# Kernel tuning notes

Hardware: AMD Instinct MI355X
Metric: run time of the kernel (lower is better)

The kernel has to match this reference:

```python
import jax, jax.numpy as jnp
import numpy as np

D = 512        # model dim
NH = 8         # heads
NL = 4         # layers
MSL = 2048     # max_seq_len for relative positional bias
ITEM_V, CATE_V, SEG_V = 100000, 1000, 2
EPS = 1e-5


def layer_norm(x, w, b):
    mu = jnp.mean(x, axis=-1, keepdims=True)
    var = jnp.mean((x - mu) ** 2, axis=-1, keepdims=True)
    return (x - mu) * jax.lax.rsqrt(var + EPS) * w + b


def setup_inputs() -> dict:
    key = jax.random.key(0)
    ks = jax.random.split(key, 16)
    B, L = 8, 1023
    inp = {
        'historical_item_ids': jax.random.randint(ks[0], (B, L), 0, ITEM_V, dtype=jnp.int32),
        'historical_cate_ids': jax.random.randint(ks[1], (B, L), 0, CATE_V, dtype=jnp.int32),
        'historical_len': jax.random.randint(ks[2], (B,), 0, L, dtype=jnp.int32),
        'target_item_id': jax.random.randint(ks[3], (B,), 0, ITEM_V, dtype=jnp.int32),
        'target_cate_id': jax.random.randint(ks[4], (B,), 0, CATE_V, dtype=jnp.int32),
        # embeddings (init std 0.02 like _init_weights)
        'item_emb': 0.02 * jax.random.normal(ks[5], (ITEM_V, D), jnp.float32),
        'cate_emb': 0.02 * jax.random.normal(ks[6], (CATE_V, D), jnp.float32),
        'seg_emb': 0.02 * jax.random.normal(ks[7], (SEG_V, D), jnp.float32),
        # per-layer stacked params
        'W1': 0.02 * jax.random.normal(ks[8], (NL, D, 4 * D), jnp.float32),
        'b1': jnp.zeros((NL, 4 * D), jnp.float32),
        'W2': 0.02 * jax.random.normal(ks[9], (NL, D, D), jnp.float32),
        'b2': jnp.zeros((NL, D), jnp.float32),
        'ln1_w': jnp.ones((NL, D), jnp.float32), 'ln1_b': jnp.zeros((NL, D), jnp.float32),
        'ln2_w': jnp.ones((NL, D), jnp.float32), 'ln2_b': jnp.zeros((NL, D), jnp.float32),
        'pos_w': 0.02 * jax.random.normal(ks[10], (NL, 2 * MSL - 1), jnp.float32),
        'lnf_w': jnp.ones((D,), jnp.float32), 'lnf_b': jnp.zeros((D,), jnp.float32),
    }
    return inp


def _forward(historical_item_ids, historical_cate_ids, historical_len,
             target_item_id, target_cate_id,
             item_emb, cate_emb, seg_emb, W1, b1, W2, b2,
             ln1_w, ln1_b, ln2_w, ln2_b, pos_w, lnf_w, lnf_b):
    B = historical_item_ids.shape[0]
    ar = jnp.arange(B)
    pad = jnp.zeros((B, 1), historical_item_ids.dtype)
    ids = jnp.concatenate([historical_item_ids, pad], axis=1).at[ar, historical_len].set(target_item_id)
    cids = jnp.concatenate([historical_cate_ids, pad], axis=1).at[ar, historical_len].set(target_cate_id)
    S = ids.shape[1]
    seg = jnp.zeros_like(ids).at[ar, historical_len].set(1)

    h = item_emb[ids] + cate_emb[cids] + seg_emb[seg]  # [B,S,D]

    # relative position bias indices: bias[i,j] = pos_w[MSL-1 + j - i]
    rel_idx = MSL - 1 + jnp.arange(S)[None, :] - jnp.arange(S)[:, None]  # [S,S]
    causal = jnp.tril(jnp.ones((S, S), h.dtype))  # multiplicative mask (mask >= 0)

    for l in range(NL):
        z = jax.nn.silu(h @ W1[l] + b1[l])  # [B,S,4D]
        u, q, k, v = jnp.split(z, 4, axis=-1)
        resh = lambda t: t.reshape(B, S, NH, D // NH).transpose(0, 2, 1, 3)  # [B,H,S,hd]
        u, q, k, v = resh(u), resh(q), resh(k), resh(v)
        bias = pos_w[l][rel_idx]  # [S,S]
        att = jax.nn.silu(jnp.einsum('bhsd,bhtd->bhst', q, k) + bias) * causal
        y = jnp.einsum('bhst,bhtd->bhsd', att, v) * u
        y = y.transpose(0, 2, 1, 3).reshape(B, S, D)
        y = layer_norm(y, ln1_w[l], ln1_b[l])
        y = y @ W2[l] + b2[l]
        h = layer_norm(y + h, ln2_w[l], ln2_b[l])  # dropout p=0 (eval)

    return layer_norm(h, lnf_w, lnf_b)


def reference(historical_item_ids, historical_cate_ids, historical_len,
              target_item_id, target_cate_id,
              item_emb, cate_emb, seg_emb, W1, b1, W2, b2,
              ln1_w, ln1_b, ln2_w, ln2_b, pos_w, lnf_w, lnf_b):
    return _forward(historical_item_ids, historical_cate_ids, historical_len,
                    target_item_id, target_cate_id,
                    item_emb, cate_emb, seg_emb, W1, b1, W2, b2,
                    ln1_w, ln1_b, ln2_w, ln2_b, pos_w, lnf_w, lnf_b)
```

## Files before the change

kernel.cpp:

```cpp
#include <hip/hip_runtime.h>
#include <cstddef>


#define D_MODEL 512
#define S_LEN 1024
#define NHEADS 8

typedef __bf16 bf16x8 __attribute__((ext_vector_type(8)));
typedef float f32x4 __attribute__((ext_vector_type(4)));
typedef unsigned short us4 __attribute__((ext_vector_type(4)));
typedef unsigned short us8 __attribute__((ext_vector_type(8)));

__device__ __forceinline__ float silu_f(float x) {
  return x / (1.f + __expf(-x));
}
__device__ __forceinline__ unsigned short f2bf(float f) {
  unsigned int u = __float_as_uint(f);
  u += 0x7FFF + ((u >> 16) & 1);
  return (unsigned short)(u >> 16);
}
__device__ __forceinline__ float bf2f(unsigned short s) {
  return __uint_as_float(((unsigned int)s) << 16);
}
__device__ __forceinline__ void gll16(const void* g, void* l) {
  __builtin_amdgcn_global_load_lds(
      (const __attribute__((address_space(1))) unsigned int*)g,
      (__attribute__((address_space(3))) unsigned int*)l, 16, 0, 0);
}

__global__ __launch_bounds__(256) void embed_kernel(
    const int* __restrict__ hist_i, const int* __restrict__ hist_c,
    const int* __restrict__ hlen, const int* __restrict__ tgt_i,
    const int* __restrict__ tgt_c, const float* __restrict__ item_emb,
    const float* __restrict__ cate_emb, const float* __restrict__ seg_emb,
    float* __restrict__ h32, unsigned short* __restrict__ hbf) {
  int bs = blockIdx.x;
  int b = bs >> 10, s = bs & 1023;
  int l = hlen[b];
  int id, cid, sg;
  if (s == l)       { id = tgt_i[b]; cid = tgt_c[b]; sg = 1; }
  else if (s < 1023){ id = hist_i[b * 1023 + s]; cid = hist_c[b * 1023 + s]; sg = 0; }
  else              { id = 0; cid = 0; sg = 0; }
  const float* ie = item_emb + (size_t)id * D_MODEL;
  const float* ce = cate_emb + (size_t)cid * D_MODEL;
  const float* se = seg_emb + (size_t)sg * D_MODEL;
  float* hr = h32 + (size_t)bs * D_MODEL;
  unsigned short* hb = hbf + (size_t)bs * D_MODEL;
  for (int d = threadIdx.x; d < D_MODEL; d += 256) {
    float v = ie[d] + ce[d] + se[d];
    hr[d] = v;
    hb[d] = f2bf(v);
  }
}

__global__ __launch_bounds__(256) void transpose_kernel(
    const float* __restrict__ W, unsigned short* __restrict__ Wt,
    int K, int N) {
  const int l = blockIdx.z;
  W += (size_t)l * K * N;
  Wt += (size_t)l * K * N;
  const int n0 = blockIdx.x * 64, k0 = blockIdx.y * 64;
  __shared__ float T[64][65];
  const int tid = threadIdx.x;
  const int rr = tid >> 4, cc = (tid & 15) * 4;
#pragma unroll
  for (int p = 0; p < 4; p++) {
    const int r = rr + p * 16;
    const float4 v = *reinterpret_cast<const float4*>(&W[(size_t)(k0 + r) * N + n0 + cc]);
    T[r][cc] = v.x; T[r][cc + 1] = v.y; T[r][cc + 2] = v.z; T[r][cc + 3] = v.w;
  }
  __syncthreads();
#pragma unroll
  for (int p = 0; p < 4; p++) {
    const int r = rr + p * 16;
    us4 o = { f2bf(T[cc + 0][r]), f2bf(T[cc + 1][r]),
              f2bf(T[cc + 2][r]), f2bf(T[cc + 3][r]) };
    *reinterpret_cast<us4*>(&Wt[(size_t)(n0 + r) * K + k0 + cc]) = o;
  }
}

template <int TM, int TN, int SWZ, int EPI_SILU, typename OutT>
__global__ __launch_bounds__(256) void mfma_gemm(
    const unsigned short* __restrict__ A, const unsigned short* __restrict__ Bt,
    const float* __restrict__ bias, OutT* __restrict__ C,
    int M, int N, int K) {
  constexpr int MI = TM / 32, NI = TN / 32;
  __shared__ unsigned short As[TM * 64];
  __shared__ unsigned short Bs[TN * 64];
  const int tid = threadIdx.x;
  const int w = tid >> 6, lane = tid & 63, lm = lane & 15, quad = lane >> 4;
  const int wm = w & 1, wn = w >> 1;
  int m0, n0;
  if (SWZ) {
    const int id = blockIdx.x;
    const int xcd = id & 7, j = id >> 3;
    m0 = (xcd * 4 + (j & 3)) * TM;
    n0 = (j >> 2) * TN;
  } else {
    m0 = blockIdx.y * TM;
    n0 = blockIdx.x * TN;
  }

  f32x4 acc[MI][NI] = {};

  for (int k0 = 0; k0 < K; k0 += 64) {
#pragma unroll
    for (int p = 0; p < TM / 32; p++) {
      const int g = p * 256 + tid;
      const int r = g >> 3;
      const int lc = (g & 7) ^ (r & 7);
      gll16(A + (size_t)(m0 + r) * K + k0 + lc * 8, &As[g * 8]);
    }
#pragma unroll
    for (int p = 0; p < TN / 32; p++) {
      const int g = p * 256 + tid;
      const int r = g >> 3;
      const int lc = (g & 7) ^ (r & 7);
      gll16(Bt + (size_t)(n0 + r) * K + k0 + lc * 8, &Bs[g * 8]);
    }
    __syncthreads();
#pragma unroll
    for (int ki = 0; ki < 2; ki++) {
      bf16x8 af[MI], bfr[NI];
#pragma unroll
      for (int mi = 0; mi < MI; mi++) {
        const int r = wm * (TM / 2) + mi * 16 + lm;
        const int p = (ki * 4 + quad) ^ (lm & 7);
        af[mi] = *reinterpret_cast<const bf16x8*>(&As[r * 64 + p * 8]);
      }
#pragma unroll
      for (int ni = 0; ni < NI; ni++) {
        const int r = wn * (TN / 2) + ni * 16 + lm;
        const int p = (ki * 4 + quad) ^ (lm & 7);
        bfr[ni] = *reinterpret_cast<const bf16x8*>(&Bs[r * 64 + p * 8]);
      }
#pragma unroll
      for (int mi = 0; mi < MI; mi++)
#pragma unroll
        for (int ni = 0; ni < NI; ni++)
          acc[mi][ni] = __builtin_amdgcn_mfma_f32_16x16x32_bf16(
              af[mi], bfr[ni], acc[mi][ni], 0, 0, 0);
    }
    __syncthreads();
  }

#pragma unroll
  for (int ni = 0; ni < NI; ni++) {
    const int n = n0 + wn * (TN / 2) + ni * 16 + lm;
    const float bv = bias[n];
#pragma unroll
    for (int mi = 0; mi < MI; mi++) {
      const int mbase = m0 + wm * (TM / 2) + mi * 16 + quad * 4;
#pragma unroll
      for (int reg = 0; reg < 4; reg++) {
        float v = acc[mi][ni][reg] + bv;
        if (EPI_SILU) v = silu_f(v);
        if constexpr (sizeof(OutT) == 2)
          C[(size_t)(mbase + reg) * N + n] = f2bf(v);
        else
          C[(size_t)(mbase + reg) * N + n] = v;
      }
    }
  }
}

#define LDR 72
__global__ __launch_bounds__(256) void attn_kernel(
    const unsigned short* __restrict__ z, const float* __restrict__ posw,
    float* __restrict__ y) {
  const int hh = blockIdx.y, b = blockIdx.z;
  __shared__ alignas(16) unsigned short Ks[64 * LDR];
  __shared__ alignas(16) unsigned short Vt[64 * LDR];
  __shared__ alignas(16) unsigned short Ps[64 * LDR];
  __shared__ float bias_s[128];
  const unsigned short* zb = z + (size_t)b * S_LEN * 2048;
  const int tid = threadIdx.x;
  const int w = tid >> 6, lane = tid & 63, lm = lane & 15, quad = lane >> 4;

#pragma unroll
  for (int phase = 0; phase < 2; phase++) {
    const int qt = phase == 0 ? (int)blockIdx.x : 15 - (int)blockIdx.x;
    const int s0 = qt * 64;
    const int srow = s0 + w * 16 + lm;

    const bf16x8 qb0 = *reinterpret_cast<const bf16x8*>(
        zb + (size_t)srow * 2048 + 512 + hh * 64 + quad * 8);
    const bf16x8 qb1 = *reinterpret_cast<const bf16x8*>(
        zb + (size_t)srow * 2048 + 512 + hh * 64 + 32 + quad * 8);

    f32x4 O[4] = {};

    for (int kt = 0; kt <= qt; kt++) {
      const int t0 = kt * 64;
      __syncthreads();
#pragma unroll
      for (int p = 0; p < 2; p++) {
        const int g = p * 256 + tid;
        const int r = g >> 3, ch = (g & 7) * 8;
        *reinterpret_cast<us8*>(&Ks[r * LDR + ch]) =
            *reinterpret_cast<const us8*>(zb + (size_t)(t0 + r) * 2048 + 1024 + hh * 64 + ch);
      }
      {
        const int t = (tid >> 4) * 4;
        const int d = (tid & 15) * 4;
        unsigned short c[4][4];
#pragma unroll
        for (int r = 0; r < 4; r++) {
          const us4 v = *reinterpret_cast<const us4*>(
              zb + (size_t)(t0 + t + r) * 2048 + 1536 + hh * 64 + d);
          c[r][0] = v.x; c[r][1] = v.y; c[r][2] = v.z; c[r][3] = v.w;
        }
        const int tb = t >> 3, ti = t & 7;
#pragma unroll
        for (int j = 0; j < 4; j++) {
          const int dd = d + j;
          us4 o = { c[0][j], c[1][j], c[2][j], c[3][j] };
          *reinterpret_cast<us4*>(&Vt[dd * LDR + ((tb ^ (dd & 7)) << 3) + ti]) = o;
        }
      }
      if (tid < 128) bias_s[tid] = posw[2047 + t0 - s0 - 63 + tid];
      __syncthreads();

#pragma unroll
      for (int tt = 0; tt < 4; tt++) {
        const bf16x8 ka0 = *reinterpret_cast<const bf16x8*>(&Ks[(tt * 16 + lm) * LDR + quad * 8]);
        const bf16x8 ka1 = *reinterpret_cast<const bf16x8*>(&Ks[(tt * 16 + lm) * LDR + 32 + quad * 8]);
        f32x4 st = {};
        st = __builtin_amdgcn_mfma_f32_16x16x32_bf16(ka0, qb0, st, 0, 0, 0);
        st = __builtin_amdgcn_mfma_f32_16x16x32_bf16(ka1, qb1, st, 0, 0, 0);
        const int bbase = 63 + tt * 16 + quad * 4 - w * 16 - lm;
        const int tq = t0 + tt * 16 + quad * 4;
        us4 pv;
        unsigned short* pp = (unsigned short*)&pv;
#pragma unroll
        for (int i = 0; i < 4; i++) {
          const float x = st[i] + bias_s[bbase + i];
          const float val = (tq + i <= srow) ? silu_f(x) : 0.f;
          pp[i] = f2bf(val);
        }
        *reinterpret_cast<us4*>(&Ps[(w * 16 + lm) * LDR + tt * 16 + quad * 4]) = pv;
      }

      const bf16x8 pa0 = *reinterpret_cast<const bf16x8*>(&Ps[(w * 16 + lm) * LDR + quad * 8]);
      const bf16x8 pa1 = *reinterpret_cast<const bf16x8*>(&Ps[(w * 16 + lm) * LDR + 32 + quad * 8]);
#pragma unroll
      for (int ct = 0; ct < 4; ct++) {
        const int d = ct * 16 + lm;
        const bf16x8 vb0 = *reinterpret_cast<const bf16x8*>(
            &Vt[d * LDR + ((quad ^ (d & 7)) << 3)]);
        const bf16x8 vb1 = *reinterpret_cast<const bf16x8*>(
            &Vt[d * LDR + (((4 + quad) ^ (d & 7)) << 3)]);
        O[ct] = __builtin_amdgcn_mfma_f32_16x16x32_bf16(pa0, vb0, O[ct], 0, 0, 0);
        O[ct] = __builtin_amdgcn_mfma_f32_16x16x32_bf16(pa1, vb1, O[ct], 0, 0, 0);
      }
    }

    {
      const int sbase = s0 + w * 16 + quad * 4;
#pragma unroll
      for (int ct = 0; ct < 4; ct++) {
        const int d = ct * 16 + lm;
#pragma unroll
        for (int i = 0; i < 4; i++) {
          const int sg = sbase + i;
          const float u = bf2f(zb[(size_t)sg * 2048 + hh * 64 + d]);
          y[((size_t)(b * S_LEN + sg)) * D_MODEL + hh * 64 + d] = O[ct][i] * u;
        }
      }
    }
  }
}

__global__ __launch_bounds__(256) void ln_kernel(
    const float* __restrict__ x, const float* __restrict__ res,
    const float* __restrict__ w, const float* __restrict__ bb,
    float* __restrict__ o32, unsigned short* __restrict__ obf) {
  const int wv = threadIdx.x >> 6, lane = threadIdx.x & 63;
  const size_t row = blockIdx.x * 4 + wv;
  const int i0 = lane * 4, i1 = 256 + lane * 4;
  float4 v0 = *reinterpret_cast<const float4*>(&x[row * D_MODEL + i0]);
  float4 v1 = *reinterpret_cast<const float4*>(&x[row * D_MODEL + i1]);
  if (res) {
    const float4 r0 = *reinterpret_cast<const float4*>(&res[row * D_MODEL + i0]);
    const float4 r1 = *reinterpret_cast<const float4*>(&res[row * D_MODEL + i1]);
    v0.x += r0.x; v0.y += r0.y; v0.z += r0.z; v0.w += r0.w;
    v1.x += r1.x; v1.y += r1.y; v1.z += r1.z; v1.w += r1.w;
  }
  float s = v0.x + v0.y + v0.z + v0.w + v1.x + v1.y + v1.z + v1.w;
  float ss = v0.x * v0.x + v0.y * v0.y + v0.z * v0.z + v0.w * v0.w +
             v1.x * v1.x + v1.y * v1.y + v1.z * v1.z + v1.w * v1.w;
#pragma unroll
  for (int off = 32; off; off >>= 1) {
    s += __shfl_down(s, off, 64);
    ss += __shfl_down(ss, off, 64);
  }
  s = __shfl(s, 0, 64);
  ss = __shfl(ss, 0, 64);
  const float mu = s * (1.f / D_MODEL);
  const float rstd = rsqrtf(ss * (1.f / D_MODEL) - mu * mu + 1e-5f);
  const float4 w0 = *reinterpret_cast<const float4*>(&w[i0]);
  const float4 w1 = *reinterpret_cast<const float4*>(&w[i1]);
  const float4 b0 = *reinterpret_cast<const float4*>(&bb[i0]);
  const float4 b1 = *reinterpret_cast<const float4*>(&bb[i1]);
  float r[8];
  r[0] = (v0.x - mu) * rstd * w0.x + b0.x;
  r[1] = (v0.y - mu) * rstd * w0.y + b0.y;
  r[2] = (v0.z - mu) * rstd * w0.z + b0.z;
  r[3] = (v0.w - mu) * rstd * w0.w + b0.w;
  r[4] = (v1.x - mu) * rstd * w1.x + b1.x;
  r[5] = (v1.y - mu) * rstd * w1.y + b1.y;
  r[6] = (v1.z - mu) * rstd * w1.z + b1.z;
  r[7] = (v1.w - mu) * rstd * w1.w + b1.w;
  if (o32) {
    *reinterpret_cast<float4*>(&o32[row * D_MODEL + i0]) = make_float4(r[0], r[1], r[2], r[3]);
    *reinterpret_cast<float4*>(&o32[row * D_MODEL + i1]) = make_float4(r[4], r[5], r[6], r[7]);
  }
  if (obf) {
    us4 q0 = { f2bf(r[0]), f2bf(r[1]), f2bf(r[2]), f2bf(r[3]) };
    us4 q1 = { f2bf(r[4]), f2bf(r[5]), f2bf(r[6]), f2bf(r[7]) };
    *reinterpret_cast<us4*>(&obf[row * D_MODEL + i0]) = q0;
    *reinterpret_cast<us4*>(&obf[row * D_MODEL + i1]) = q1;
  }
}

extern "C" void kernel_launch(void* const* d_in, const int* in_sizes, int n_in,
                              void* d_out, int out_size, void* d_ws, size_t ws_size,
                              hipStream_t stream) {
  const int* hist_i = (const int*)d_in[0];
  const int* hist_c = (const int*)d_in[1];
  const int* hlen   = (const int*)d_in[2];
  const int* tgt_i  = (const int*)d_in[3];
  const int* tgt_c  = (const int*)d_in[4];
  const float* item_emb = (const float*)d_in[5];
  const float* cate_emb = (const float*)d_in[6];
  const float* seg_emb  = (const float*)d_in[7];
  const float* W1   = (const float*)d_in[8];
  const float* b1   = (const float*)d_in[9];
  const float* W2   = (const float*)d_in[10];
  const float* b2   = (const float*)d_in[11];
  const float* ln1w = (const float*)d_in[12];
  const float* ln1b = (const float*)d_in[13];
  const float* ln2w = (const float*)d_in[14];
  const float* ln2b = (const float*)d_in[15];
  const float* posw = (const float*)d_in[16];
  const float* lnfw = (const float*)d_in[17];
  const float* lnfb = (const float*)d_in[18];
  float* out = (float*)d_out;

  char* ws = (char*)d_ws;
  float*          h32 = (float*)(ws);
  unsigned short* hbf = (unsigned short*)(ws + (16u << 20));
  unsigned short* zbf = (unsigned short*)(ws + (24u << 20));
  unsigned short* ybf = (unsigned short*)(ws + (56u << 20));
  float*          yat = (float*)(ws + (64u << 20));
  float*          t32 = yat;
  unsigned short* W1t = (unsigned short*)(ws + (80u << 20));
  unsigned short* W2t = (unsigned short*)(ws + (88u << 20));

  const int ROWS = 8 * S_LEN;

  transpose_kernel<<<dim3(2048 / 64, 512 / 64, 4), 256, 0, stream>>>(W1, W1t, 512, 2048);
  transpose_kernel<<<dim3(512 / 64, 512 / 64, 4), 256, 0, stream>>>(W2, W2t, 512, 512);
  embed_kernel<<<ROWS, 256, 0, stream>>>(hist_i, hist_c, hlen, tgt_i, tgt_c,
                                         item_emb, cate_emb, seg_emb, h32, hbf);
  for (int l = 0; l < 4; l++) {
    mfma_gemm<256, 128, 1, 1, unsigned short><<<512, 256, 0, stream>>>(
        hbf, W1t + (size_t)l * 2048 * 512, b1 + (size_t)l * 2048, zbf, ROWS, 2048, 512);
    attn_kernel<<<dim3(8, NHEADS, 8), 256, 0, stream>>>(
        zbf, posw + (size_t)l * 4095, yat);
    ln_kernel<<<ROWS / 4, 256, 0, stream>>>(yat, nullptr, ln1w + l * 512, ln1b + l * 512,
                                            nullptr, ybf);
    mfma_gemm<64, 64, 0, 0, float><<<dim3(512 / 64, ROWS / 64), 256, 0, stream>>>(
        ybf, W2t + (size_t)l * 512 * 512, b2 + (size_t)l * 512, t32, ROWS, 512, 512);
    ln_kernel<<<ROWS / 4, 256, 0, stream>>>(t32, h32, ln2w + l * 512, ln2b + l * 512,
                                            h32, hbf);
  }
  ln_kernel<<<ROWS / 4, 256, 0, stream>>>(h32, nullptr, lnfw, lnfb, out, nullptr);
}
```

Before: 819.2 us.

## Store intermediates in bf16, split attention blocks, retile GEMMs, swizzle K loads

The attention output and the W2 GEMM output become bf16 instead of fp32, and the layernorm kernel is templated to read bf16 input with 8-element vectorized loads. This roughly halves the traffic of those intermediate tensors. The attention grid is doubled so each block handles one query tile instead of a paired two-phase loop. K tiles are loaded through an async global-to-LDS copy with an XOR swizzle. The W1 GEMM tile shrinks to 128x128 with a generalized XCD swizzle, and the W2 GEMM uses 64x128 tiles. Rounding intermediates to bf16 adds precision loss, and the single-tile attention blocks bring back load imbalance across the causal tiles.

```diff
diff --git a/kernel.cpp b/kernel.cpp
--- a/kernel.cpp
+++ b/kernel.cpp
@@ -94,8 +94,9 @@
   if (SWZ) {
     const int id = blockIdx.x;
     const int xcd = id & 7, j = id >> 3;
-    m0 = (xcd * 4 + (j & 3)) * TM;
-    n0 = (j >> 2) * TN;
+    const int mPerX = (M / TM) >> 3;
+    m0 = (xcd * mPerX + (j % mPerX)) * TM;
+    n0 = (j / mPerX) * TN;
   } else {
     m0 = blockIdx.y * TM;
     n0 = blockIdx.x * TN;
@@ -167,128 +168,137 @@
 #define LDR 72
 __global__ __launch_bounds__(256) void attn_kernel(
     const unsigned short* __restrict__ z, const float* __restrict__ posw,
-    float* __restrict__ y) {
+    unsigned short* __restrict__ y) {
+  const int qt = 15 - (int)blockIdx.x;
   const int hh = blockIdx.y, b = blockIdx.z;
-  __shared__ alignas(16) unsigned short Ks[64 * LDR];
+  const int s0 = qt * 64;
+  __shared__ alignas(16) unsigned short Ks[64 * 64];
   __shared__ alignas(16) unsigned short Vt[64 * LDR];
   __shared__ alignas(16) unsigned short Ps[64 * LDR];
   __shared__ float bias_s[128];
   const unsigned short* zb = z + (size_t)b * S_LEN * 2048;
   const int tid = threadIdx.x;
   const int w = tid >> 6, lane = tid & 63, lm = lane & 15, quad = lane >> 4;
-
-#pragma unroll
-  for (int phase = 0; phase < 2; phase++) {
-    const int qt = phase == 0 ? (int)blockIdx.x : 15 - (int)blockIdx.x;
-    const int s0 = qt * 64;
-    const int srow = s0 + w * 16 + lm;
-
-    const bf16x8 qb0 = *reinterpret_cast<const bf16x8*>(
-        zb + (size_t)srow * 2048 + 512 + hh * 64 + quad * 8);
-    const bf16x8 qb1 = *reinterpret_cast<const bf16x8*>(
-        zb + (size_t)srow * 2048 + 512 + hh * 64 + 32 + quad * 8);
-
-    f32x4 O[4] = {};
-
-    for (int kt = 0; kt <= qt; kt++) {
-      const int t0 = kt * 64;
-      __syncthreads();
-#pragma unroll
-      for (int p = 0; p < 2; p++) {
-        const int g = p * 256 + tid;
-        const int r = g >> 3, ch = (g & 7) * 8;
-        *reinterpret_cast<us8*>(&Ks[r * LDR + ch]) =
-            *reinterpret_cast<const us8*>(zb + (size_t)(t0 + r) * 2048 + 1024 + hh * 64 + ch);
-      }
-      {
-        const int t = (tid >> 4) * 4;
-        const int d = (tid & 15) * 4;
-        unsigned short c[4][4];
-#pragma unroll
-        for (int r = 0; r < 4; r++) {
-          const us4 v = *reinterpret_cast<const us4*>(
-              zb + (size_t)(t0 + t + r) * 2048 + 1536 + hh * 64 + d);
-          c[r][0] = v.x; c[r][1] = v.y; c[r][2] = v.z; c[r][3] = v.w;
-        }
-        const int tb = t >> 3, ti = t & 7;
-#pragma unroll
-        for (int j = 0; j < 4; j++) {
-          const int dd = d + j;
-          us4 o = { c[0][j], c[1][j], c[2][j], c[3][j] };
-          *reinterpret_cast<us4*>(&Vt[dd * LDR + ((tb ^ (dd & 7)) << 3) + ti]) = o;
-        }
-      }
-      if (tid < 128) bias_s[tid] = posw[2047 + t0 - s0 - 63 + tid];
-      __syncthreads();
-
-#pragma unroll
-      for (int tt = 0; tt < 4; tt++) {
-        const bf16x8 ka0 = *reinterpret_cast<const bf16x8*>(&Ks[(tt * 16 + lm) * LDR + quad * 8]);
-        const bf16x8 ka1 = *reinterpret_cast<const bf16x8*>(&Ks[(tt * 16 + lm) * LDR + 32 + quad * 8]);
-        f32x4 st = {};
-        st = __builtin_amdgcn_mfma_f32_16x16x32_bf16(ka0, qb0, st, 0, 0, 0);
-        st = __builtin_amdgcn_mfma_f32_16x16x32_bf16(ka1, qb1, st, 0, 0, 0);
-        const int bbase = 63 + tt * 16 + quad * 4 - w * 16 - lm;
-        const int tq = t0 + tt * 16 + quad * 4;
-        us4 pv;
-        unsigned short* pp = (unsigned short*)&pv;
-#pragma unroll
-        for (int i = 0; i < 4; i++) {
-          const float x = st[i] + bias_s[bbase + i];
-          const float val = (tq + i <= srow) ? silu_f(x) : 0.f;
-          pp[i] = f2bf(val);
-        }
-        *reinterpret_cast<us4*>(&Ps[(w * 16 + lm) * LDR + tt * 16 + quad * 4]) = pv;
-      }
-
-      const bf16x8 pa0 = *reinterpret_cast<const bf16x8*>(&Ps[(w * 16 + lm) * LDR + quad * 8]);
-      const bf16x8 pa1 = *reinterpret_cast<const bf16x8*>(&Ps[(w * 16 + lm) * LDR + 32 + quad * 8]);
-#pragma unroll
-      for (int ct = 0; ct < 4; ct++) {
-        const int d = ct * 16 + lm;
-        const bf16x8 vb0 = *reinterpret_cast<const bf16x8*>(
-            &Vt[d * LDR + ((quad ^ (d & 7)) << 3)]);
-        const bf16x8 vb1 = *reinterpret_cast<const bf16x8*>(
-            &Vt[d * LDR + (((4 + quad) ^ (d & 7)) << 3)]);
-        O[ct] = __builtin_amdgcn_mfma_f32_16x16x32_bf16(pa0, vb0, O[ct], 0, 0, 0);
-        O[ct] = __builtin_amdgcn_mfma_f32_16x16x32_bf16(pa1, vb1, O[ct], 0, 0, 0);
-      }
-    }
-
+  const int srow = s0 + w * 16 + lm;
+
+  const bf16x8 qb0 = *reinterpret_cast<const bf16x8*>(
+      zb + (size_t)srow * 2048 + 512 + hh * 64 + quad * 8);
+  const bf16x8 qb1 = *reinterpret_cast<const bf16x8*>(
+      zb + (size_t)srow * 2048 + 512 + hh * 64 + 32 + quad * 8);
+
+  f32x4 O[4] = {};
+
+  for (int kt = 0; kt <= qt; kt++) {
+    const int t0 = kt * 64;
+    __syncthreads();
+#pragma unroll
+    for (int p = 0; p < 2; p++) {
+      const int g = p * 256 + tid;
+      const int r = g >> 3;
+      const int lc = (g & 7) ^ (r & 7);
+      gll16(zb + (size_t)(t0 + r) * 2048 + 1024 + hh * 64 + lc * 8, &Ks[g * 8]);
+    }
     {
-      const int sbase = s0 + w * 16 + quad * 4;
-#pragma unroll
-      for (int ct = 0; ct < 4; ct++) {
-        const int d = ct * 16 + lm;
-#pragma unroll
-        for (int i = 0; i < 4; i++) {
-          const int sg = sbase + i;
-          const float u = bf2f(zb[(size_t)sg * 2048 + hh * 64 + d]);
-          y[((size_t)(b * S_LEN + sg)) * D_MODEL + hh * 64 + d] = O[ct][i] * u;
-        }
-      }
-    }
-  }
-}
-
+      const int t = (tid >> 4) * 4;
+      const int d = (tid & 15) * 4;
+      unsigned short c[4][4];
+#pragma unroll
+      for (int r = 0; r < 4; r++) {
+        const us4 v = *reinterpret_cast<const us4*>(
+            zb + (size_t)(t0 + t + r) * 2048 + 1536 + hh * 64 + d);
+        c[r][0] = v.x; c[r][1] = v.y; c[r][2] = v.z; c[r][3] = v.w;
+      }
+      const int tb = t >> 3, ti = t & 7;
+#pragma unroll
+      for (int j = 0; j < 4; j++) {
+        const int dd = d + j;
+        us4 o = { c[0][j], c[1][j], c[2][j], c[3][j] };
+        *reinterpret_cast<us4*>(&Vt[dd * LDR + ((tb ^ (dd & 7)) << 3) + ti]) = o;
+      }
+    }
+    if (tid < 128) bias_s[tid] = posw[2047 + t0 - s0 - 63 + tid];
+    __syncthreads();
+
+#pragma unroll
+    for (int tt = 0; tt < 4; tt++) {
+      const int r = tt * 16 + lm;
+      const int p0 = quad ^ (r & 7);
+      const int p1 = (4 + quad) ^ (r & 7);
+      const bf16x8 ka0 = *reinterpret_cast<const bf16x8*>(&Ks[r * 64 + p0 * 8]);
+      const bf16x8 ka1 = *reinterpret_cast<const bf16x8*>(&Ks[r * 64 + p1 * 8]);
+      f32x4 st = {};
+      st = __builtin_amdgcn_mfma_f32_16x16x32_bf16(ka0, qb0, st, 0, 0, 0);
+      st = __builtin_amdgcn_mfma_f32_16x16x32_bf16(ka1, qb1, st, 0, 0, 0);
+      const int bbase = 63 + tt * 16 + quad * 4 - w * 16 - lm;
+      const int tq = t0 + tt * 16 + quad * 4;
+      us4 pv;
+      unsigned short* pp = (unsigned short*)&pv;
+#pragma unroll
+      for (int i = 0; i < 4; i++) {
+        const float x = st[i] + bias_s[bbase + i];
+        const float val = (tq + i <= srow) ? silu_f(x) : 0.f;
+        pp[i] = f2bf(val);
+      }
+      *reinterpret_cast<us4*>(&Ps[(w * 16 + lm) * LDR + tt * 16 + quad * 4]) = pv;
+    }
+
+    const bf16x8 pa0 = *reinterpret_cast<const bf16x8*>(&Ps[(w * 16 + lm) * LDR + quad * 8]);
+    const bf16x8 pa1 = *reinterpret_cast<const bf16x8*>(&Ps[(w * 16 + lm) * LDR + 32 + quad * 8]);
+#pragma unroll
+    for (int ct = 0; ct < 4; ct++) {
+      const int d = ct * 16 + lm;
+      const bf16x8 vb0 = *reinterpret_cast<const bf16x8*>(
+          &Vt[d * LDR + ((quad ^ (d & 7)) << 3)]);
+      const bf16x8 vb1 = *reinterpret_cast<const bf16x8*>(
+          &Vt[d * LDR + (((4 + quad) ^ (d & 7)) << 3)]);
+      O[ct] = __builtin_amdgcn_mfma_f32_16x16x32_bf16(pa0, vb0, O[ct], 0, 0, 0);
+      O[ct] = __builtin_amdgcn_mfma_f32_16x16x32_bf16(pa1, vb1, O[ct], 0, 0, 0);
+    }
+  }
+
+  {
+    const int sbase = s0 + w * 16 + quad * 4;
+#pragma unroll
+    for (int ct = 0; ct < 4; ct++) {
+      const int d = ct * 16 + lm;
+#pragma unroll
+      for (int i = 0; i < 4; i++) {
+        const int sg = sbase + i;
+        const float u = bf2f(zb[(size_t)sg * 2048 + hh * 64 + d]);
+        y[((size_t)(b * S_LEN + sg)) * D_MODEL + hh * 64 + d] = f2bf(O[ct][i] * u);
+      }
+    }
+  }
+}
+
+template <typename XT>
 __global__ __launch_bounds__(256) void ln_kernel(
-    const float* __restrict__ x, const float* __restrict__ res,
+    const XT* __restrict__ x, const float* __restrict__ res,
     const float* __restrict__ w, const float* __restrict__ bb,
     float* __restrict__ o32, unsigned short* __restrict__ obf) {
   const int wv = threadIdx.x >> 6, lane = threadIdx.x & 63;
   const size_t row = blockIdx.x * 4 + wv;
-  const int i0 = lane * 4, i1 = 256 + lane * 4;
-  float4 v0 = *reinterpret_cast<const float4*>(&x[row * D_MODEL + i0]);
-  float4 v1 = *reinterpret_cast<const float4*>(&x[row * D_MODEL + i1]);
+  const int c0 = lane * 8;
+  float v[8];
+  if constexpr (sizeof(XT) == 2) {
+    const us8 u = *reinterpret_cast<const us8*>(&x[row * D_MODEL + c0]);
+#pragma unroll
+    for (int i = 0; i < 8; i++) v[i] = bf2f(u[i]);
+  } else {
+    const float4 a = *reinterpret_cast<const float4*>(&x[row * D_MODEL + c0]);
+    const float4 c = *reinterpret_cast<const float4*>(&x[row * D_MODEL + c0 + 4]);
+    v[0] = a.x; v[1] = a.y; v[2] = a.z; v[3] = a.w;
+    v[4] = c.x; v[5] = c.y; v[6] = c.z; v[7] = c.w;
+  }
   if (res) {
-    const float4 r0 = *reinterpret_cast<const float4*>(&res[row * D_MODEL + i0]);
-    const float4 r1 = *reinterpret_cast<const float4*>(&res[row * D_MODEL + i1]);
-    v0.x += r0.x; v0.y += r0.y; v0.z += r0.z; v0.w += r0.w;
-    v1.x += r1.x; v1.y += r1.y; v1.z += r1.z; v1.w += r1.w;
-  }
-  float s = v0.x + v0.y + v0.z + v0.w + v1.x + v1.y + v1.z + v1.w;
-  float ss = v0.x * v0.x + v0.y * v0.y + v0.z * v0.z + v0.w * v0.w +
-             v1.x * v1.x + v1.y * v1.y + v1.z * v1.z + v1.w * v1.w;
+    const float4 r0 = *reinterpret_cast<const float4*>(&res[row * D_MODEL + c0]);
+    const float4 r1 = *reinterpret_cast<const float4*>(&res[row * D_MODEL + c0 + 4]);
+    v[0] += r0.x; v[1] += r0.y; v[2] += r0.z; v[3] += r0.w;
+    v[4] += r1.x; v[5] += r1.y; v[6] += r1.z; v[7] += r1.w;
+  }
+  float s = 0.f, ss = 0.f;
+#pragma unroll
+  for (int i = 0; i < 8; i++) { s += v[i]; ss += v[i] * v[i]; }
 #pragma unroll
   for (int off = 32; off; off >>= 1) {
     s += __shfl_down(s, off, 64);
@@ -298,28 +308,27 @@
   ss = __shfl(ss, 0, 64);
   const float mu = s * (1.f / D_MODEL);
   const float rstd = rsqrtf(ss * (1.f / D_MODEL) - mu * mu + 1e-5f);
-  const float4 w0 = *reinterpret_cast<const float4*>(&w[i0]);
-  const float4 w1 = *reinterpret_cast<const float4*>(&w[i1]);
-  const float4 b0 = *reinterpret_cast<const float4*>(&bb[i0]);
-  const float4 b1 = *reinterpret_cast<const float4*>(&bb[i1]);
+  const float4 w0 = *reinterpret_cast<const float4*>(&w[c0]);
+  const float4 w1 = *reinterpret_cast<const float4*>(&w[c0 + 4]);
+  const float4 b0 = *reinterpret_cast<const float4*>(&bb[c0]);
+  const float4 b1 = *reinterpret_cast<const float4*>(&bb[c0 + 4]);
   float r[8];
-  r[0] = (v0.x - mu) * rstd * w0.x + b0.x;
-  r[1] = (v0.y - mu) * rstd * w0.y + b0.y;
-  r[2] = (v0.z - mu) * rstd * w0.z + b0.z;
-  r[3] = (v0.w - mu) * rstd * w0.w + b0.w;
-  r[4] = (v1.x - mu) * rstd * w1.x + b1.x;
-  r[5] = (v1.y - mu) * rstd * w1.y + b1.y;
-  r[6] = (v1.z - mu) * rstd * w1.z + b1.z;
-  r[7] = (v1.w - mu) * rstd * w1.w + b1.w;
+  r[0] = (v[0] - mu) * rstd * w0.x + b0.x;
+  r[1] = (v[1] - mu) * rstd * w0.y + b0.y;
+  r[2] = (v[2] - mu) * rstd * w0.z + b0.z;
+  r[3] = (v[3] - mu) * rstd * w0.w + b0.w;
+  r[4] = (v[4] - mu) * rstd * w1.x + b1.x;
+  r[5] = (v[5] - mu) * rstd * w1.y + b1.y;
+  r[6] = (v[6] - mu) * rstd * w1.z + b1.z;
+  r[7] = (v[7] - mu) * rstd * w1.w + b1.w;
   if (o32) {
-    *reinterpret_cast<float4*>(&o32[row * D_MODEL + i0]) = make_float4(r[0], r[1], r[2], r[3]);
-    *reinterpret_cast<float4*>(&o32[row * D_MODEL + i1]) = make_float4(r[4], r[5], r[6], r[7]);
+    *reinterpret_cast<float4*>(&o32[row * D_MODEL + c0]) = make_float4(r[0], r[1], r[2], r[3]);
+    *reinterpret_cast<float4*>(&o32[row * D_MODEL + c0 + 4]) = make_float4(r[4], r[5], r[6], r[7]);
   }
   if (obf) {
-    us4 q0 = { f2bf(r[0]), f2bf(r[1]), f2bf(r[2]), f2bf(r[3]) };
-    us4 q1 = { f2bf(r[4]), f2bf(r[5]), f2bf(r[6]), f2bf(r[7]) };
-    *reinterpret_cast<us4*>(&obf[row * D_MODEL + i0]) = q0;
-    *reinterpret_cast<us4*>(&obf[row * D_MODEL + i1]) = q1;
+    us8 q = { f2bf(r[0]), f2bf(r[1]), f2bf(r[2]), f2bf(r[3]),
+              f2bf(r[4]), f2bf(r[5]), f2bf(r[6]), f2bf(r[7]) };
+    *reinterpret_cast<us8*>(&obf[row * D_MODEL + c0]) = q;
   }
 }
 
@@ -352,8 +361,8 @@
   unsigned short* hbf = (unsigned short*)(ws + (16u << 20));
   unsigned short* zbf = (unsigned short*)(ws + (24u << 20));
   unsigned short* ybf = (unsigned short*)(ws + (56u << 20));
-  float*          yat = (float*)(ws + (64u << 20));
-  float*          t32 = yat;
+  unsigned short* yab = (unsigned short*)(ws + (64u << 20));
+  unsigned short* tbf = yab;
   unsigned short* W1t = (unsigned short*)(ws + (80u << 20));
   unsigned short* W2t = (unsigned short*)(ws + (88u << 20));
 
@@ -364,16 +373,16 @@
   embed_kernel<<<ROWS, 256, 0, stream>>>(hist_i, hist_c, hlen, tgt_i, tgt_c,
                                          item_emb, cate_emb, seg_emb, h32, hbf);
   for (int l = 0; l < 4; l++) {
-    mfma_gemm<256, 128, 1, 1, unsigned short><<<512, 256, 0, stream>>>(
+    mfma_gemm<128, 128, 1, 1, unsigned short><<<1024, 256, 0, stream>>>(
         hbf, W1t + (size_t)l * 2048 * 512, b1 + (size_t)l * 2048, zbf, ROWS, 2048, 512);
-    attn_kernel<<<dim3(8, NHEADS, 8), 256, 0, stream>>>(
-        zbf, posw + (size_t)l * 4095, yat);
-    ln_kernel<<<ROWS / 4, 256, 0, stream>>>(yat, nullptr, ln1w + l * 512, ln1b + l * 512,
-                                            nullptr, ybf);
-    mfma_gemm<64, 64, 0, 0, float><<<dim3(512 / 64, ROWS / 64), 256, 0, stream>>>(
-        ybf, W2t + (size_t)l * 512 * 512, b2 + (size_t)l * 512, t32, ROWS, 512, 512);
-    ln_kernel<<<ROWS / 4, 256, 0, stream>>>(t32, h32, ln2w + l * 512, ln2b + l * 512,
-                                            h32, hbf);
-  }
-  ln_kernel<<<ROWS / 4, 256, 0, stream>>>(h32, nullptr, lnfw, lnfb, out, nullptr);
-}
+    attn_kernel<<<dim3(16, NHEADS, 8), 256, 0, stream>>>(
+        zbf, posw + (size_t)l * 4095, yab);
+    ln_kernel<unsigned short><<<ROWS / 4, 256, 0, stream>>>(
+        yab, nullptr, ln1w + l * 512, ln1b + l * 512, nullptr, ybf);
+    mfma_gemm<64, 128, 0, 0, unsigned short><<<dim3(512 / 128, ROWS / 64), 256, 0, stream>>>(
+        ybf, W2t + (size_t)l * 512 * 512, b2 + (size_t)l * 512, tbf, ROWS, 512, 512);
+    ln_kernel<unsigned short><<<ROWS / 4, 256, 0, stream>>>(
+        tbf, h32, ln2w + l * 512, ln2b + l * 512, h32, hbf);
+  }
+  ln_kernel<float><<<ROWS / 4, 256, 0, stream>>>(h32, nullptr, lnfw, lnfb, out, nullptr);
+}
```

Result: slower. 878.2 us (+7.2%).
